# Kernel optimization log

Measured on AMD Instinct MI355X. Metric: run time of the kernel, lower is better.

The kernel has to match this reference:

```python
import jax, jax.numpy as jnp
import numpy as np
import math

B, LQ, LK = 8, 1024, 1024
DQ = DK = DV = DOUT = 512
H = 8
DH = DOUT // H
EPS = 1e-5


def _ln(x, g, b):
    m = jnp.mean(x, -1, keepdims=True)
    var = jnp.mean((x - m) ** 2, -1, keepdims=True)
    return (x - m) * jax.lax.rsqrt(var + EPS) * g + b


def setup_inputs() -> dict:
    key = jax.random.key(0)
    ks = jax.random.split(key, 13)
    s = 0.02
    return {
        "q": jax.random.normal(ks[0], (B, LQ, DQ), jnp.float32),
        "k": jax.random.normal(ks[1], (B, LK, DK), jnp.float32),
        "v": jax.random.normal(ks[2], (B, LK, DV), jnp.float32),
        "mask": jax.random.randint(ks[3], (B, LK), 0, 2) > 0,  # True = masked
        "Wq": jax.random.normal(ks[4], (DOUT, DQ), jnp.float32) * s,
        "Wk": jax.random.normal(ks[5], (DOUT, DK), jnp.float32) * s,
        "Wv": jax.random.normal(ks[6], (DOUT, DV), jnp.float32) * s,
        "Wo": jax.random.normal(ks[7], (DOUT, DOUT), jnp.float32) * s,
        "bo": jnp.zeros((DOUT,), jnp.float32),
        "g1": jnp.ones((DOUT,), jnp.float32),
        "b1": jnp.zeros((DOUT,), jnp.float32),
        "g2": jnp.ones((DOUT,), jnp.float32),
        "b2": jnp.zeros((DOUT,), jnp.float32),
    }


def reference(q, k, v, mask, Wq, Wk, Wv, Wo, bo, g1, b1, g2, b2):
    qp = q @ Wq.T  # [B,Lq,D]
    kp = k @ Wk.T  # [B,Lk,D]
    vp = v @ Wv.T  # [B,Lk,D]

    # split heads: chunk(num_heads, -1) -> head h = contiguous slice of size DH
    qh = qp.reshape(B, LQ, H, DH)
    kh = kp.reshape(B, LK, H, DH)
    vh = vp.reshape(B, LK, H, DH)

    # NOTE: module divides by sqrt(dim_out), not sqrt(head_dim)
    logits = jnp.einsum("bqhd,bkhd->bhqk", qh, kh) / math.sqrt(DOUT)
    logits = jnp.where(mask[:, None, None, :], -jnp.inf, logits)
    A = jax.nn.softmax(logits, axis=-1)
    A = jnp.where(jnp.isnan(A), 0.0, A)  # masked_fill(isnan, 0)

    attn = jnp.einsum("bhqk,bkhd->bqhd", A, vh).reshape(B, LQ, DOUT)

    out = _ln(qp + attn, g1, b1)
    out = _ln(out + jax.nn.relu(out @ Wo.T + bo), g2, b2)
    return out
```

## Files before the change

### kernel.cpp

```cpp
#include <hip/hip_runtime.h>
#include <math.h>
#include <stdint.h>

#define NB 8
#define SEQ 1024
#define DMODEL 512
#define NH 8
#define HD 64
#define R_TOT (NB * SEQ)

typedef __attribute__((ext_vector_type(8))) short bf16x8;
typedef __attribute__((ext_vector_type(4))) float f32x4;

__device__ __forceinline__ short f2b(float x) {
    uint32_t u = __float_as_uint(x);
    u += 0x7FFF + ((u >> 16) & 1);
    return (short)(u >> 16);
}
__device__ __forceinline__ float b2f(short s) {
    return __uint_as_float(((uint32_t)(uint16_t)s) << 16);
}
__device__ __forceinline__ uint32_t cvtpk_bf16(float lo, float hi) {
    uint32_t r;
    asm("v_cvt_pk_bf16_f32 %0, %1, %2" : "=v"(r) : "v"(lo), "v"(hi));
    return r;
}
__device__ __forceinline__ float exp2_hw(float x) {
    float r;
    asm("v_exp_f32 %0, %1" : "=v"(r) : "v"(x));
    return r;
}

#define GLD_LDS16(g, l)                                                        \
    __builtin_amdgcn_global_load_lds(                                          \
        (const __attribute__((address_space(1))) uint32_t*)(g),                \
        (__attribute__((address_space(3))) uint32_t*)(l), 16, 0, 0)

__device__ __forceinline__ void xcd_swizzle(int& bx, int& by, int& bz) {
    const int gx = gridDim.x, gy = gridDim.y;
    const int nwg = gx * gy * gridDim.z;
    int id = (blockIdx.z * gy + blockIdx.y) * gx + blockIdx.x;
    int lg = (id & 7) * (nwg >> 3) + (id >> 3);
    bx = lg % gx;
    int tmp = lg / gx;
    by = tmp % gy;
    bz = tmp / gy;
}

#define N4B (R_TOT * DMODEL / 4)
#define N4W (DMODEL * DMODEL / 4)

__global__ __launch_bounds__(256)
void cvt_all(const float* __restrict__ q, const float* __restrict__ k, const float* __restrict__ v,
             const float* __restrict__ wq, const float* __restrict__ wk,
             const float* __restrict__ wv, const float* __restrict__ wo,
             short* dq, short* dk, short* dv, short* dwq, short* dwk, short* dwv, short* dwo)
{
    long i = (long)blockIdx.x * 256 + threadIdx.x;
    const float* s; short* d; long off;
    if (i < (long)N4B)          { s = q;  d = dq;  off = i; }
    else if (i < 2L * N4B)      { s = k;  d = dk;  off = i - N4B; }
    else if (i < 3L * N4B)      { s = v;  d = dv;  off = i - 2L * N4B; }
    else {
        long j = i - 3L * N4B;
        int  w = (int)(j >> 16);
        off = j & (N4W - 1);
        s = (w == 0) ? wq : (w == 1) ? wk : (w == 2) ? wv : wo;
        d = (w == 0) ? dwq : (w == 1) ? dwk : (w == 2) ? dwv : dwo;
    }
    float4 x = ((const float4*)s)[off];
    short4 o;
    o.x = f2b(x.x); o.y = f2b(x.y); o.z = f2b(x.z); o.w = f2b(x.w);
    ((short4*)d)[off] = o;
}

#define GBM 128
#define GBN 64
#define GBK 64

__device__ __forceinline__ void gemm_core(
    const short* __restrict__ A, const short* __restrict__ Bm,
    const float* __restrict__ bias, const short* __restrict__ resid,
    short* __restrict__ C,
    int N, int m0, int n0, int relu, float oscale,
    short (*As)[GBM * GBK], short (*Bs)[GBN * GBK])
{
    const int tid = threadIdx.x;
    const int l   = tid & 63, w = tid >> 6;
    const int l15 = l & 15,  l4 = l >> 4;
    const int wrow = w >> 1, wcol = w & 1;
    const int K = 512;

    f32x4 acc[4][2] = {};

    auto stageA = [&](int t, int buf) {
        #pragma unroll
        for (int j = 0; j < 4; ++j) {
            int ch  = tid + j * 256;
            int row = ch >> 3;
            int so  = (((ch & 7) * 16) ^ ((row & 7) << 4)) >> 1;
            GLD_LDS16(A + (size_t)(m0 + row) * K + t * GBK + so, &As[buf][ch * 8]);
        }
    };
    auto stageB = [&](int t, int buf) {
        #pragma unroll
        for (int j = 0; j < 2; ++j) {
            int ch  = tid + j * 256;
            int row = ch >> 3;
            int so  = (((ch & 7) * 16) ^ ((row & 7) << 4)) >> 1;
            GLD_LDS16(Bm + (size_t)(n0 + row) * K + t * GBK + so, &Bs[buf][ch * 8]);
        }
    };

    stageA(0, 0); stageB(0, 0);
    __syncthreads();

    for (int t = 0; t < 8; ++t) {
        const int cur = t & 1;
        if (t + 1 < 8) { stageA(t + 1, cur ^ 1); stageB(t + 1, cur ^ 1); }
        __builtin_amdgcn_s_setprio(1);
        #pragma unroll
        for (int kk = 0; kk < 2; ++kk) {
            bf16x8 af[4], bfr[2];
            #pragma unroll
            for (int mi = 0; mi < 4; ++mi) {
                int row = wrow * 64 + mi * 16 + l15;
                af[mi] = *(const bf16x8*)((char*)&As[cur][row * GBK] +
                                          ((kk * 64 + l4 * 16) ^ ((row & 7) << 4)));
            }
            #pragma unroll
            for (int ni = 0; ni < 2; ++ni) {
                int row = wcol * 32 + ni * 16 + l15;
                bfr[ni] = *(const bf16x8*)((char*)&Bs[cur][row * GBK] +
                                           ((kk * 64 + l4 * 16) ^ ((row & 7) << 4)));
            }
            #pragma unroll
            for (int mi = 0; mi < 4; ++mi)
                #pragma unroll
                for (int ni = 0; ni < 2; ++ni)
                    acc[mi][ni] = __builtin_amdgcn_mfma_f32_16x16x32_bf16(af[mi], bfr[ni], acc[mi][ni], 0, 0, 0);
        }
        __builtin_amdgcn_s_setprio(0);
        __syncthreads();
    }

    #pragma unroll
    for (int mi = 0; mi < 4; ++mi) {
        #pragma unroll
        for (int ni = 0; ni < 2; ++ni) {
            int col = n0 + wcol * 32 + ni * 16 + l15;
            float bb = bias ? bias[col] : 0.0f;
            #pragma unroll
            for (int r = 0; r < 4; ++r) {
                int row = m0 + wrow * 64 + mi * 16 + l4 * 4 + r;
                float vv = (acc[mi][ni][r] + bb) * oscale;
                if (relu) vv = fmaxf(vv, 0.0f);
                if (resid) vv += b2f(resid[(size_t)row * N + col]);
                C[(size_t)row * N + col] = f2b(vv);
            }
        }
    }
}

__global__ __launch_bounds__(256)
void proj3(const short* __restrict__ qb, const short* __restrict__ kb,
           const short* __restrict__ vb, const short* __restrict__ wq,
           const short* __restrict__ wv,
           short* __restrict__ qpb, short* __restrict__ vtb, float kscale)
{
    __shared__ short As[2][GBM * GBK];
    __shared__ short Bs[2][GBN * GBK];
    const size_t WSZ  = (size_t)DMODEL * DMODEL;
    const size_t SLOT = (size_t)R_TOT * DMODEL;

    int id = blockIdx.x;
    int lg = (id & 7) * 192 + (id >> 3);

    const short *A, *Bm; short* C; int N, m0, n0; float os = 1.0f;
    if (lg < 1024) {
        int bz  = lg >> 9;
        int rem = lg & 511;
        m0 = (rem >> 3) * GBM;
        n0 = (rem & 7) * GBN;
        A  = bz ? kb : qb;
        Bm = wq + bz * WSZ;
        C  = qpb + bz * SLOT;
        N  = DMODEL;
        os = bz ? kscale : 1.0f;
    } else {
        int r2  = lg - 1024;
        int b   = r2 >> 6;
        int rem = r2 & 63;
        m0 = (rem >> 4) * GBM;
        n0 = (rem & 15) * GBN;
        A  = wv;
        Bm = vb + (long)b * SEQ * DMODEL;
        C  = vtb + (long)b * DMODEL * SEQ;
        N  = SEQ;
    }
    gemm_core(A, Bm, nullptr, nullptr, C, N, m0, n0, 0, os, As, Bs);
}

__global__ __launch_bounds__(256)
void outproj(const short* __restrict__ y, const short* __restrict__ wo,
             const float* __restrict__ bias, short* __restrict__ z)
{
    __shared__ short As[2][GBM * GBK];
    __shared__ short Bs[2][GBN * GBK];
    int bx, by, bz;
    xcd_swizzle(bx, by, bz);
    gemm_core(y, wo, bias, y, z, DMODEL, by * GBM, bx * GBN, 1, 1.0f, As, Bs);
}

__global__ __launch_bounds__(512)
void attn_mfma9(const short* __restrict__ qp, const short* __restrict__ kp,
                const short* __restrict__ vt, const int* __restrict__ mask,
                short* __restrict__ attn)
{
    __shared__ short Kb[2][2][64 * 64];
    __shared__ short Vb[2][2][64 * 64];
    __shared__ __align__(16) char Ps[8 * 2048];

    const int tid = threadIdx.x;
    const int l   = tid & 63, w = tid >> 6;
    const int l15 = l & 15,  l4 = l >> 4;
    int qb_, h, b;
    xcd_swizzle(qb_, h, b);
    const int qrow = qb_ * 128 + w * 16 + l15;
    const size_t baseqk = ((size_t)b * SEQ) * DMODEL + h * HD;
    const size_t basev  = ((size_t)b * DMODEL + h * HD) * SEQ;

    const int ch  = tid;
    const int row = ch >> 3;
    const int so  = ((((ch & 7) * 16) ^ ((row & 7) << 4)) >> 1);
    const short* kph = kp + baseqk;
    const short* vth = vt + basev;
    const int*   mrow = mask + b * SEQ;

#define STAGE(t, bufi) do {                                                                   \
        GLD_LDS16(kph + (size_t)((t) * 128 + row) * DMODEL + so,      &Kb[bufi][0][ch * 8]);  \
        GLD_LDS16(kph + (size_t)((t) * 128 + 64 + row) * DMODEL + so, &Kb[bufi][1][ch * 8]);  \
        GLD_LDS16(vth + (size_t)row * SEQ + (t) * 128 + so,           &Vb[bufi][0][ch * 8]);  \
        GLD_LDS16(vth + (size_t)row * SEQ + (t) * 128 + 64 + so,      &Vb[bufi][1][ch * 8]);  \
    } while (0)

    const int swk   = (l15 & 7) << 4;
    const int kOff0 = l15 * 128 + ((l4 * 16) ^ swk);
    const int kOff1 = l15 * 128 + ((64 + l4 * 16) ^ swk);
    int pwOff[4];
    #pragma unroll
    for (int c = 0; c < 4; ++c)
        pwOff[c] = (l15 * 128 + c * 32 + l4 * 8) ^ swk;
    const int prOff0 = (l15 * 128 + l4 * 16) ^ swk;
    const int prOff1 = (l15 * 128 + 64 + l4 * 16) ^ swk;

    bf16x8 qf0, qf1;
    {
        const short* qr = qp + baseqk + (size_t)qrow * DMODEL + l4 * 8;
        qf0 = *(const bf16x8*)qr;
        qf1 = *(const bf16x8*)(qr + 32);
    }
    const bf16x8 ones = {0x3F80, 0x3F80, 0x3F80, 0x3F80, 0x3F80, 0x3F80, 0x3F80, 0x3F80};

    STAGE(0, 0);
    __syncthreads();

    f32x4 oacc[4] = {};
    f32x4 osum = {};
    char* myPs = Ps + w * 2048;

    for (int t = 0; t < 8; ++t) {
        const int cur = t & 1;
        if (t < 7) STAGE(t + 1, cur ^ 1);

        int4 mreg[2][4];
        #pragma unroll
        for (int hf = 0; hf < 2; ++hf)
            #pragma unroll
            for (int c = 0; c < 4; ++c)
                mreg[hf][c] = *(const int4*)&mrow[t * 128 + hf * 64 + c * 16 + l4 * 4];

        #pragma unroll
        for (int hf = 0; hf < 2; ++hf) {
            f32x4 s[4];
            __builtin_amdgcn_s_setprio(1);
            #pragma unroll
            for (int c = 0; c < 4; ++c) {
                const char* kbase = (const char*)&Kb[cur][hf][0] + c * 2048;
                bf16x8 kf0 = *(const bf16x8*)(kbase + kOff0);
                bf16x8 kf1 = *(const bf16x8*)(kbase + kOff1);
                f32x4 zz = {};
                zz = __builtin_amdgcn_mfma_f32_16x16x32_bf16(kf0, qf0, zz, 0, 0, 0);
                zz = __builtin_amdgcn_mfma_f32_16x16x32_bf16(kf1, qf1, zz, 0, 0, 0);
                s[c] = zz;
            }
            __builtin_amdgcn_s_setprio(0);

            float p[16];
            #pragma unroll
            for (int c = 0; c < 4; ++c) {
                int4 mi = mreg[hf][c];
                p[c * 4 + 0] = exp2_hw(mi.x ? -1.0e30f : s[c][0]);
                p[c * 4 + 1] = exp2_hw(mi.y ? -1.0e30f : s[c][1]);
                p[c * 4 + 2] = exp2_hw(mi.z ? -1.0e30f : s[c][2]);
                p[c * 4 + 3] = exp2_hw(mi.w ? -1.0e30f : s[c][3]);
            }

            #pragma unroll
            for (int c = 0; c < 4; ++c) {
                uint2 u;
                u.x = cvtpk_bf16(p[c * 4 + 0], p[c * 4 + 1]);
                u.y = cvtpk_bf16(p[c * 4 + 2], p[c * 4 + 3]);
                *(uint2*)(myPs + pwOff[c]) = u;
            }
            bf16x8 pf0 = *(const bf16x8*)(myPs + prOff0);
            bf16x8 pf1 = *(const bf16x8*)(myPs + prOff1);

            __builtin_amdgcn_s_setprio(1);
            osum = __builtin_amdgcn_mfma_f32_16x16x32_bf16(ones, pf0, osum, 0, 0, 0);
            osum = __builtin_amdgcn_mfma_f32_16x16x32_bf16(ones, pf1, osum, 0, 0, 0);
            #pragma unroll
            for (int db = 0; db < 4; ++db) {
                const char* vbase = (const char*)&Vb[cur][hf][0] + db * 2048;
                bf16x8 vf0 = *(const bf16x8*)(vbase + kOff0);
                bf16x8 vf1 = *(const bf16x8*)(vbase + kOff1);
                oacc[db] = __builtin_amdgcn_mfma_f32_16x16x32_bf16(vf0, pf0, oacc[db], 0, 0, 0);
                oacc[db] = __builtin_amdgcn_mfma_f32_16x16x32_bf16(vf1, pf1, oacc[db], 0, 0, 0);
            }
            __builtin_amdgcn_s_setprio(0);
        }
        __syncthreads();
    }
#undef STAGE

    float inv = (osum[0] > 0.0f) ? 1.0f / osum[0] : 0.0f;
    #pragma unroll
    for (int db = 0; db < 4; ++db) {
        const size_t eoff = baseqk + (size_t)qrow * DMODEL + db * 16 + l4 * 4;
        short4 qv = *(const short4*)(qp + eoff);
        short4 o;
        o.x = f2b(oacc[db][0] * inv + b2f(qv.x));
        o.y = f2b(oacc[db][1] * inv + b2f(qv.y));
        o.z = f2b(oacc[db][2] * inv + b2f(qv.z));
        o.w = f2b(oacc[db][3] * inv + b2f(qv.w));
        *(short4*)(attn + eoff) = o;
    }
}

__global__ __launch_bounds__(256)
void ln_one(const short* __restrict__ X, const float* __restrict__ g,
            const float* __restrict__ beta, short* __restrict__ outb,
            float* __restrict__ outf)
{
    const int row  = blockIdx.x * 4 + (threadIdx.x >> 6);
    const int lane = threadIdx.x & 63;
    const size_t off = (size_t)row * DMODEL + lane * 8;
    bf16x8 xv = *(const bf16x8*)&X[off];
    float x[8], s = 0.0f, sq = 0.0f;
    #pragma unroll
    for (int i = 0; i < 8; ++i) {
        x[i] = b2f(xv[i]);
        s += x[i];
        sq += x[i] * x[i];
    }
    #pragma unroll
    for (int o = 1; o < 64; o <<= 1) {
        s  += __shfl_xor(s,  o);
        sq += __shfl_xor(sq, o);
    }
    const float mean = s * (1.0f / DMODEL);
    const float var  = sq * (1.0f / DMODEL) - mean * mean;
    const float rs   = rsqrtf(var + 1e-5f);
    float4 g0 = *(const float4*)&g[lane * 8];
    float4 g1 = *(const float4*)&g[lane * 8 + 4];
    float4 b0 = *(const float4*)&beta[lane * 8];
    float4 b1 = *(const float4*)&beta[lane * 8 + 4];
    float gg[8] = {g0.x, g0.y, g0.z, g0.w, g1.x, g1.y, g1.z, g1.w};
    float bb[8] = {b0.x, b0.y, b0.z, b0.w, b1.x, b1.y, b1.z, b1.w};
    float y[8];
    #pragma unroll
    for (int i = 0; i < 8; ++i)
        y[i] = (x[i] - mean) * rs * gg[i] + bb[i];
    if (outb) {
        bf16x8 o;
        #pragma unroll
        for (int i = 0; i < 8; ++i) o[i] = f2b(y[i]);
        *(bf16x8*)&outb[off] = o;
    } else {
        float4 o0 = {y[0], y[1], y[2], y[3]};
        float4 o1 = {y[4], y[5], y[6], y[7]};
        *(float4*)&outf[off] = o0;
        *(float4*)&outf[off + 4] = o1;
    }
}

extern "C" void kernel_launch(void* const* d_in, const int* in_sizes, int n_in,
                              void* d_out, int out_size, void* d_ws, size_t ws_size,
                              hipStream_t stream)
{
    const float* q    = (const float*)d_in[0];
    const float* k    = (const float*)d_in[1];
    const float* v    = (const float*)d_in[2];
    const int*   mask = (const int*)  d_in[3];
    const float* Wq   = (const float*)d_in[4];
    const float* Wk   = (const float*)d_in[5];
    const float* Wv   = (const float*)d_in[6];
    const float* Wo   = (const float*)d_in[7];
    const float* bo   = (const float*)d_in[8];
    const float* g1   = (const float*)d_in[9];
    const float* b1   = (const float*)d_in[10];
    const float* g2   = (const float*)d_in[11];
    const float* bt2  = (const float*)d_in[12];
    float* out = (float*)d_out;

    short* ws = (short*)d_ws;
    const size_t WSZ  = (size_t)DMODEL * DMODEL;
    const size_t SLOT = (size_t)R_TOT * DMODEL;
    short* wq  = ws;
    short* wk  = ws + WSZ;
    short* wv  = ws + 2 * WSZ;
    short* wo  = ws + 3 * WSZ;
    short* qb  = ws + 4 * WSZ;
    short* kb  = qb + SLOT;
    short* vb  = kb + SLOT;
    short* qpb = vb + SLOT;
    short* kpb = qpb + SLOT;
    short* vtb = kpb + SLOT;
    short* at  = qb;
    short* y   = kb;
    short* z   = vb;

    const int nCvtBlocks = (3 * N4B + 4 * N4W) / 256;
    cvt_all<<<nCvtBlocks, 256, 0, stream>>>(q, k, v, Wq, Wk, Wv, Wo,
                                            qb, kb, vb, wq, wk, wv, wo);

    const float kscale = 0.06375871530f;

    proj3<<<1536, 256, 0, stream>>>(qb, kb, vb, wq, wv, qpb, vtb, kscale);

    attn_mfma9<<<dim3(SEQ / 128, NH, NB), 512, 0, stream>>>(qpb, kpb, vtb, mask, at);

    ln_one<<<R_TOT / 4, 256, 0, stream>>>(at, g1, b1, y, nullptr);

    outproj<<<dim3(DMODEL / GBN, R_TOT / GBM, 1), 256, 0, stream>>>(y, wo, bo, z);

    ln_one<<<R_TOT / 4, 256, 0, stream>>>(z, g2, bt2, nullptr, out);
}
```

Baseline: 92.79 us.

## Triple-buffer attention K/V tiles with 64-key steps and vmcnt waits

Replaces the double-buffered 128-key stages with a three-deep ring of 64-key K/V tiles, prefetching two stages ahead. Each step waits on explicit vmcnt counts plus a raw barrier instead of a full __syncthreads, so later async loads stay in flight. The mask row is also staged into shared memory once rather than read from global each iteration. The loop now has twice as many barriers, and correctness relies on the hand-set waitcnt values lining up with the number of outstanding async loads.

```diff
diff --git a/kernel.cpp b/kernel.cpp
--- a/kernel.cpp
+++ b/kernel.cpp
@@ -30,6 +30,7 @@
     asm("v_exp_f32 %0, %1" : "=v"(r) : "v"(x));
     return r;
 }
+#define WAITV(N) __builtin_amdgcn_s_waitcnt(0xF70 | (N))
 
 #define GLD_LDS16(g, l)                                                        \
     __builtin_amdgcn_global_load_lds(                                          \
@@ -213,13 +214,14 @@
 }
 
 __global__ __launch_bounds__(512)
-void attn_mfma9(const short* __restrict__ qp, const short* __restrict__ kp,
-                const short* __restrict__ vt, const int* __restrict__ mask,
-                short* __restrict__ attn)
-{
-    __shared__ short Kb[2][2][64 * 64];
-    __shared__ short Vb[2][2][64 * 64];
+void attn_mfma10(const short* __restrict__ qp, const short* __restrict__ kp,
+                 const short* __restrict__ vt, const int* __restrict__ mask,
+                 short* __restrict__ attn)
+{
+    __shared__ short Kb[3][64 * 64];
+    __shared__ short Vb[3][64 * 64];
     __shared__ __align__(16) char Ps[8 * 2048];
+    __shared__ __align__(16) int  Mk[SEQ];
 
     const int tid = threadIdx.x;
     const int l   = tid & 63, w = tid >> 6;
@@ -235,13 +237,10 @@
     const int so  = ((((ch & 7) * 16) ^ ((row & 7) << 4)) >> 1);
     const short* kph = kp + baseqk;
     const short* vth = vt + basev;
-    const int*   mrow = mask + b * SEQ;
-
-#define STAGE(t, bufi) do {                                                                   \
-        GLD_LDS16(kph + (size_t)((t) * 128 + row) * DMODEL + so,      &Kb[bufi][0][ch * 8]);  \
-        GLD_LDS16(kph + (size_t)((t) * 128 + 64 + row) * DMODEL + so, &Kb[bufi][1][ch * 8]);  \
-        GLD_LDS16(vth + (size_t)row * SEQ + (t) * 128 + so,           &Vb[bufi][0][ch * 8]);  \
-        GLD_LDS16(vth + (size_t)row * SEQ + (t) * 128 + 64 + so,      &Vb[bufi][1][ch * 8]);  \
+
+#define STG(t, bi) do {                                                          \
+        GLD_LDS16(kph + (size_t)((t) * 64 + row) * DMODEL + so, &Kb[bi][ch * 8]); \
+        GLD_LDS16(vth + (size_t)row * SEQ + (t) * 64 + so,      &Vb[bi][ch * 8]); \
     } while (0)
 
     const int swk   = (l15 & 7) << 4;
@@ -262,76 +261,73 @@
     }
     const bf16x8 ones = {0x3F80, 0x3F80, 0x3F80, 0x3F80, 0x3F80, 0x3F80, 0x3F80, 0x3F80};
 
-    STAGE(0, 0);
+    if (tid < 256) GLD_LDS16(mask + b * SEQ + tid * 4, &Mk[tid * 4]);
+    STG(0, 0);
+    STG(1, 1);
     __syncthreads();
 
     f32x4 oacc[4] = {};
     f32x4 osum = {};
     char* myPs = Ps + w * 2048;
 
-    for (int t = 0; t < 8; ++t) {
-        const int cur = t & 1;
-        if (t < 7) STAGE(t + 1, cur ^ 1);
-
-        int4 mreg[2][4];
-        #pragma unroll
-        for (int hf = 0; hf < 2; ++hf)
-            #pragma unroll
-            for (int c = 0; c < 4; ++c)
-                mreg[hf][c] = *(const int4*)&mrow[t * 128 + hf * 64 + c * 16 + l4 * 4];
-
-        #pragma unroll
-        for (int hf = 0; hf < 2; ++hf) {
-            f32x4 s[4];
-            __builtin_amdgcn_s_setprio(1);
-            #pragma unroll
-            for (int c = 0; c < 4; ++c) {
-                const char* kbase = (const char*)&Kb[cur][hf][0] + c * 2048;
-                bf16x8 kf0 = *(const bf16x8*)(kbase + kOff0);
-                bf16x8 kf1 = *(const bf16x8*)(kbase + kOff1);
-                f32x4 zz = {};
-                zz = __builtin_amdgcn_mfma_f32_16x16x32_bf16(kf0, qf0, zz, 0, 0, 0);
-                zz = __builtin_amdgcn_mfma_f32_16x16x32_bf16(kf1, qf1, zz, 0, 0, 0);
-                s[c] = zz;
-            }
-            __builtin_amdgcn_s_setprio(0);
-
-            float p[16];
-            #pragma unroll
-            for (int c = 0; c < 4; ++c) {
-                int4 mi = mreg[hf][c];
-                p[c * 4 + 0] = exp2_hw(mi.x ? -1.0e30f : s[c][0]);
-                p[c * 4 + 1] = exp2_hw(mi.y ? -1.0e30f : s[c][1]);
-                p[c * 4 + 2] = exp2_hw(mi.z ? -1.0e30f : s[c][2]);
-                p[c * 4 + 3] = exp2_hw(mi.w ? -1.0e30f : s[c][3]);
-            }
-
-            #pragma unroll
-            for (int c = 0; c < 4; ++c) {
-                uint2 u;
-                u.x = cvtpk_bf16(p[c * 4 + 0], p[c * 4 + 1]);
-                u.y = cvtpk_bf16(p[c * 4 + 2], p[c * 4 + 3]);
-                *(uint2*)(myPs + pwOff[c]) = u;
-            }
-            bf16x8 pf0 = *(const bf16x8*)(myPs + prOff0);
-            bf16x8 pf1 = *(const bf16x8*)(myPs + prOff1);
-
-            __builtin_amdgcn_s_setprio(1);
-            osum = __builtin_amdgcn_mfma_f32_16x16x32_bf16(ones, pf0, osum, 0, 0, 0);
-            osum = __builtin_amdgcn_mfma_f32_16x16x32_bf16(ones, pf1, osum, 0, 0, 0);
-            #pragma unroll
-            for (int db = 0; db < 4; ++db) {
-                const char* vbase = (const char*)&Vb[cur][hf][0] + db * 2048;
-                bf16x8 vf0 = *(const bf16x8*)(vbase + kOff0);
-                bf16x8 vf1 = *(const bf16x8*)(vbase + kOff1);
-                oacc[db] = __builtin_amdgcn_mfma_f32_16x16x32_bf16(vf0, pf0, oacc[db], 0, 0, 0);
-                oacc[db] = __builtin_amdgcn_mfma_f32_16x16x32_bf16(vf1, pf1, oacc[db], 0, 0, 0);
-            }
-            __builtin_amdgcn_s_setprio(0);
-        }
-        __syncthreads();
-    }
-#undef STAGE
+    #pragma unroll
+    for (int t = 0; t < 16; ++t) {
+        const int bi = t % 3;
+        if (t + 2 < 16) STG(t + 2, (t + 2) % 3);
+        if (t <= 13)      WAITV(4);
+        else if (t == 14) WAITV(2);
+        else              WAITV(0);
+        __builtin_amdgcn_s_barrier();
+
+        f32x4 s[4];
+        __builtin_amdgcn_s_setprio(1);
+        #pragma unroll
+        for (int c = 0; c < 4; ++c) {
+            const char* kbase = (const char*)&Kb[bi][0] + c * 2048;
+            bf16x8 kf0 = *(const bf16x8*)(kbase + kOff0);
+            bf16x8 kf1 = *(const bf16x8*)(kbase + kOff1);
+            f32x4 zz = {};
+            zz = __builtin_amdgcn_mfma_f32_16x16x32_bf16(kf0, qf0, zz, 0, 0, 0);
+            zz = __builtin_amdgcn_mfma_f32_16x16x32_bf16(kf1, qf1, zz, 0, 0, 0);
+            s[c] = zz;
+        }
+        __builtin_amdgcn_s_setprio(0);
+
+        float p[16];
+        #pragma unroll
+        for (int c = 0; c < 4; ++c) {
+            int4 mi = *(const int4*)&Mk[t * 64 + c * 16 + l4 * 4];
+            p[c * 4 + 0] = exp2_hw(mi.x ? -1.0e30f : s[c][0]);
+            p[c * 4 + 1] = exp2_hw(mi.y ? -1.0e30f : s[c][1]);
+            p[c * 4 + 2] = exp2_hw(mi.z ? -1.0e30f : s[c][2]);
+            p[c * 4 + 3] = exp2_hw(mi.w ? -1.0e30f : s[c][3]);
+        }
+
+        #pragma unroll
+        for (int c = 0; c < 4; ++c) {
+            uint2 u;
+            u.x = cvtpk_bf16(p[c * 4 + 0], p[c * 4 + 1]);
+            u.y = cvtpk_bf16(p[c * 4 + 2], p[c * 4 + 3]);
+            *(uint2*)(myPs + pwOff[c]) = u;
+        }
+        bf16x8 pf0 = *(const bf16x8*)(myPs + prOff0);
+        bf16x8 pf1 = *(const bf16x8*)(myPs + prOff1);
+
+        __builtin_amdgcn_s_setprio(1);
+        osum = __builtin_amdgcn_mfma_f32_16x16x32_bf16(ones, pf0, osum, 0, 0, 0);
+        osum = __builtin_amdgcn_mfma_f32_16x16x32_bf16(ones, pf1, osum, 0, 0, 0);
+        #pragma unroll
+        for (int db = 0; db < 4; ++db) {
+            const char* vbase = (const char*)&Vb[bi][0] + db * 2048;
+            bf16x8 vf0 = *(const bf16x8*)(vbase + kOff0);
+            bf16x8 vf1 = *(const bf16x8*)(vbase + kOff1);
+            oacc[db] = __builtin_amdgcn_mfma_f32_16x16x32_bf16(vf0, pf0, oacc[db], 0, 0, 0);
+            oacc[db] = __builtin_amdgcn_mfma_f32_16x16x32_bf16(vf1, pf1, oacc[db], 0, 0, 0);
+        }
+        __builtin_amdgcn_s_setprio(0);
+        __builtin_amdgcn_s_barrier();
+    }
+#undef STG
 
     float inv = (osum[0] > 0.0f) ? 1.0f / osum[0] : 0.0f;
     #pragma unroll
@@ -438,7 +434,7 @@
 
     proj3<<<1536, 256, 0, stream>>>(qb, kb, vb, wq, wv, qpb, vtb, kscale);
 
-    attn_mfma9<<<dim3(SEQ / 128, NH, NB), 512, 0, stream>>>(qpb, kpb, vtb, mask, at);
+    attn_mfma10<<<dim3(SEQ / 128, NH, NB), 512, 0, stream>>>(qpb, kpb, vtb, mask, at);
 
     ln_one<<<R_TOT / 4, 256, 0, stream>>>(at, g1, b1, y, nullptr);
 
```

Result: no change. 92.82 us (+0.0%).
